# Optimization experiments

Measured on AMD Instinct MI355X. Metric: run time of the kernel, lower is better.

Reference implementation:

```python
import jax, jax.numpy as jnp
import numpy as np

N_NODES = 50000


def _gcn_norm(edge_index, num_nodes):
    # add self loops, compute symmetric normalization D^-1/2 (A+I) D^-1/2
    loops = jnp.arange(num_nodes, dtype=edge_index.dtype)
    row = jnp.concatenate([edge_index[0], loops])
    col = jnp.concatenate([edge_index[1], loops])
    deg = jax.ops.segment_sum(jnp.ones_like(row, dtype=jnp.float32), col,
                              num_segments=num_nodes)
    dinv = jnp.where(deg > 0, jax.lax.rsqrt(deg), 0.0)
    norm = dinv[row] * dinv[col]  # [E']
    return row, col, norm


def _gcn_conv(x, W, b, row, col, norm, num_nodes):
    h = x @ W                       # [N, out] transform first (smaller dim)
    msg = h[row] * norm[:, None]    # gather along source nodes  [E', out]
    agg = jax.ops.segment_sum(msg, col, num_segments=num_nodes)  # scatter-add
    return agg + b


def setup_inputs() -> dict:
    key = jax.random.key(0)
    k1, k2, k3, k4 = jax.random.split(key, 4)
    x = jax.random.normal(k1, (N_NODES, 128), dtype=jnp.float32)
    edge_index = jax.random.randint(k2, (2, 800000), 0, N_NODES, dtype=jnp.int64)
    W1 = jax.random.normal(k3, (128, 128), dtype=jnp.float32) * (1.0 / np.sqrt(128))
    b1 = jnp.zeros((128,), dtype=jnp.float32)
    W2 = jax.random.normal(k4, (128, 16), dtype=jnp.float32) * (1.0 / np.sqrt(128))
    b2 = jnp.zeros((16,), dtype=jnp.float32)
    return {"x": x, "edge_index": edge_index, "W1": W1, "b1": b1, "W2": W2, "b2": b2}


def reference(x, edge_index, W1, b1, W2, b2):
    n = x.shape[0]
    row, col, norm = _gcn_norm(edge_index, n)
    h = _gcn_conv(x, W1, b1, row, col, norm, n)
    h = jax.nn.relu(h)
    h = _gcn_conv(h, W2, b2, row, col, norm, n)
    return jax.nn.log_softmax(h, axis=1)
```

## Files before the change

### kernel.cpp

```cpp
#include <hip/hip_runtime.h>
#include <math.h>

constexpr int N  = 50000;
constexpr int E  = 800000;
constexpr int F1 = 128;
constexpr int F2 = 16;
constexpr int BSHIFT  = 8;
constexpr int NBUCKET = (N + 255) >> BSHIFT;
constexpr int CHUNK   = 2048;
constexpr int CAP     = 6144;

typedef unsigned short ushort_t;
typedef unsigned char  uchar_t;
typedef __bf16 bf16x8 __attribute__((ext_vector_type(8)));
typedef float  f32x4  __attribute__((ext_vector_type(4)));

static __device__ __forceinline__ float blo(unsigned u) { return __uint_as_float(u << 16); }
static __device__ __forceinline__ float bhi(unsigned u) { return __uint_as_float(u & 0xffff0000u); }
static __device__ __forceinline__ ushort_t to_bf(float f) { __bf16 h = (__bf16)f; return *(ushort_t*)&h; }
static __device__ __forceinline__ uchar_t to_fp8(float f) {
    return (uchar_t)(__builtin_amdgcn_cvt_pk_fp8_f32(f, f, 0, false) & 0xff);
}

__global__ __launch_bounds__(256) void k_scatterP(const int* __restrict__ row,
                                                  const int* __restrict__ col,
                                                  int* __restrict__ cursor,
                                                  unsigned* __restrict__ P,
                                                  const float* __restrict__ W1,
                                                  const float* __restrict__ W2,
                                                  ushort_t* __restrict__ W1t,
                                                  ushort_t* __restrict__ W2t) {
    __shared__ int hist[NBUCKET];
    __shared__ int cur[NBUCKET];
    int t = threadIdx.x;
    if (t < NBUCKET) hist[t] = 0;
    __syncthreads();
    int base = blockIdx.x * CHUNK;
#pragma unroll
    for (int i = 0; i < CHUNK / 256; ++i) {
        int e = base + i * 256 + t;
        if (e < E) atomicAdd(&hist[col[e] >> BSHIFT], 1);
    }
    __syncthreads();
    if (t < NBUCKET) cur[t] = t * CAP + atomicAdd(&cursor[t], hist[t]);
    __syncthreads();
#pragma unroll
    for (int i = 0; i < CHUNK / 256; ++i) {
        int e = base + i * 256 + t;
        if (e < E) {
            int c = col[e];
            int pos = atomicAdd(&cur[c >> BSHIFT], 1);
            P[pos] = ((unsigned)row[e] << BSHIFT) | (unsigned)(c & 255);
        }
    }

    int gi = blockIdx.x * 256 + t;
    if (gi < F1 * F1) {
        int k = gi >> 7, n = gi & 127;
        W1t[n * F1 + k] = to_bf(W1[gi]);
    }
    if (gi < F1 * F2) {
        int k = gi >> 4, n = gi & 15;
        W2t[n * F1 + k] = to_bf(W2[gi]);
    }
}

__global__ __launch_bounds__(512) void k_binFinal(const unsigned* __restrict__ P,
                                                  const int* __restrict__ cursor,
                                                  ushort_t* __restrict__ csr16,
                                                  int* __restrict__ seg_start,
                                                  int* __restrict__ counts,
                                                  float* __restrict__ dinv) {
    __shared__ unsigned eb[CAP];
    __shared__ int cnt[256];
    __shared__ int cur[256];
    __shared__ int wtot[4];
    int t = threadIdx.x;
    int b = blockIdx.x;
    int lo = b << BSHIFT;
    int n_nodes = min(256, N - lo);
    int m = cursor[b];
    if (t < 256) cnt[t] = 0;
    __syncthreads();
    const unsigned* Pb = P + (size_t)b * CAP;
    for (int k = t; k < m; k += 512) {
        unsigned u = Pb[k];
        eb[k] = u;
        atomicAdd(&cnt[u & 255], 1);
    }
    __syncthreads();
    int lane = t & 63, wid = t >> 6;
    int v = 0, incl = 0;
    if (t < 256) {
        v = cnt[t];
        incl = v;
#pragma unroll
        for (int d = 1; d < 64; d <<= 1) {
            int u = __shfl_up(incl, d, 64);
            if (lane >= d) incl += u;
        }
        if (lane == 63) wtot[wid] = incl;
    }
    __syncthreads();
    if (t < 256) {
        int wb = 0;
        for (int w = 0; w < wid; ++w) wb += wtot[w];
        int o = b * CAP + wb + incl - v;
        cur[t] = o;
        if (t < n_nodes) {
            seg_start[lo + t] = o;
            counts[lo + t] = v;
            dinv[lo + t] = rsqrtf((float)v + 1.f);
        }
    }
    __syncthreads();
    for (int k = t; k < m; k += 512) {
        unsigned u = eb[k];
        int pos = atomicAdd(&cur[u & 255], 1);
        csr16[pos] = (ushort_t)(u >> BSHIFT);
    }
}

__global__ __launch_bounds__(256) void k_gemm1_mfma(const float* __restrict__ x,
                                                    const ushort_t* __restrict__ W1t,
                                                    const float* __restrict__ dinv,
                                                    uchar_t* __restrict__ h1q) {
    __shared__ ushort_t Wl[F1 * 136];
    int t = threadIdx.x;
    for (int i = t; i < F1 * 16; i += 256) {
        int n = i >> 4, c = (i & 15) * 8;
        *(int4*)&Wl[n * 136 + c] = *(const int4*)&W1t[n * F1 + c];
    }
    __syncthreads();

    int lane = t & 63, wv = t >> 6;
    int quad = lane >> 4, l15 = lane & 15;
    int arow = blockIdx.x * 64 + wv * 16 + l15;
    int rclamp = min(arow, N - 1);
    f32x4 acc[8] = {};

#pragma unroll
    for (int kk = 0; kk < 4; ++kk) {
        int k0 = kk * 32 + quad * 8;
        const float* xp = x + (size_t)rclamp * F1 + k0;
        float4 u0 = *(const float4*)xp;
        float4 u1 = *(const float4*)(xp + 4);
        bf16x8 a;
        a[0] = (__bf16)u0.x; a[1] = (__bf16)u0.y; a[2] = (__bf16)u0.z; a[3] = (__bf16)u0.w;
        a[4] = (__bf16)u1.x; a[5] = (__bf16)u1.y; a[6] = (__bf16)u1.z; a[7] = (__bf16)u1.w;
#pragma unroll
        for (int ct = 0; ct < 8; ++ct) {
            bf16x8 b = *(const bf16x8*)&Wl[(ct * 16 + l15) * 136 + k0];
            acc[ct] = __builtin_amdgcn_mfma_f32_16x16x32_bf16(a, b, acc[ct], 0, 0, 0);
        }
    }

    int orow0 = blockIdx.x * 64 + wv * 16 + quad * 4;
#pragma unroll
    for (int r = 0; r < 4; ++r) {
        int orow = orow0 + r;
        if (orow < N) {
            float d = dinv[orow];
#pragma unroll
            for (int ct = 0; ct < 8; ++ct)
                h1q[(size_t)orow * F1 + ct * 16 + l15] = to_fp8(acc[ct][r] * d);
        }
    }
}

__global__ __launch_bounds__(256) void k_gather1(const uchar_t* __restrict__ h1q,
                                                 const int* __restrict__ seg_start,
                                                 const int* __restrict__ counts,
                                                 const ushort_t* __restrict__ csr16,
                                                 const float* __restrict__ dinv,
                                                 const float* __restrict__ b1,
                                                 ushort_t* __restrict__ h1rb) {
    int c = (blockIdx.x * 256 + threadIdx.x) >> 6;
    int lane = threadIdx.x & 63;
    if (c >= N) return;
    int s = seg_start[c], e = s + counts[c];
    float ax = 0.f, ay = 0.f;
    int k = s;
    for (; k + 4 <= e; k += 4) {
        int r0 = csr16[k], r1 = csr16[k + 1], r2 = csr16[k + 2], r3 = csr16[k + 3];
        unsigned u0 = ((const ushort_t*)(h1q + (size_t)r0 * F1))[lane];
        unsigned u1 = ((const ushort_t*)(h1q + (size_t)r1 * F1))[lane];
        unsigned u2 = ((const ushort_t*)(h1q + (size_t)r2 * F1))[lane];
        unsigned u3 = ((const ushort_t*)(h1q + (size_t)r3 * F1))[lane];
        ax += (__builtin_amdgcn_cvt_f32_fp8(u0, 0) + __builtin_amdgcn_cvt_f32_fp8(u1, 0)) +
              (__builtin_amdgcn_cvt_f32_fp8(u2, 0) + __builtin_amdgcn_cvt_f32_fp8(u3, 0));
        ay += (__builtin_amdgcn_cvt_f32_fp8(u0, 1) + __builtin_amdgcn_cvt_f32_fp8(u1, 1)) +
              (__builtin_amdgcn_cvt_f32_fp8(u2, 1) + __builtin_amdgcn_cvt_f32_fp8(u3, 1));
    }
    for (; k < e; ++k) {
        unsigned u = ((const ushort_t*)(h1q + (size_t)csr16[k] * F1))[lane];
        ax += __builtin_amdgcn_cvt_f32_fp8(u, 0);
        ay += __builtin_amdgcn_cvt_f32_fp8(u, 1);
    }
    unsigned us = ((const ushort_t*)(h1q + (size_t)c * F1))[lane];
    ax += __builtin_amdgcn_cvt_f32_fp8(us, 0);
    ay += __builtin_amdgcn_cvt_f32_fp8(us, 1);
    float dc = dinv[c];
    float2 bb = ((const float2*)b1)[lane];
    float o0 = fmaxf(fmaf(dc, ax, bb.x), 0.f);
    float o1 = fmaxf(fmaf(dc, ay, bb.y), 0.f);
    unsigned pw = (unsigned)to_bf(o0) | ((unsigned)to_bf(o1) << 16);
    ((unsigned*)(h1rb + (size_t)c * F1))[lane] = pw;
}

__global__ __launch_bounds__(256) void k_gemm2_mfma(const ushort_t* __restrict__ h1rb,
                                                    const ushort_t* __restrict__ W2t,
                                                    const float* __restrict__ dinv,
                                                    ushort_t* __restrict__ h2s) {
    int t = threadIdx.x, lane = t & 63, wv = t >> 6;
    int quad = lane >> 4, l15 = lane & 15;
    int arow = blockIdx.x * 64 + wv * 16 + l15;
    int rclamp = min(arow, N - 1);
    f32x4 acc = {};
#pragma unroll
    for (int kk = 0; kk < 4; ++kk) {
        int k0 = kk * 32 + quad * 8;
        bf16x8 a = *(const bf16x8*)(h1rb + (size_t)rclamp * F1 + k0);
        bf16x8 b = *(const bf16x8*)(W2t + l15 * F1 + k0);
        acc = __builtin_amdgcn_mfma_f32_16x16x32_bf16(a, b, acc, 0, 0, 0);
    }
    int orow0 = blockIdx.x * 64 + wv * 16 + quad * 4;
#pragma unroll
    for (int r = 0; r < 4; ++r) {
        int orow = orow0 + r;
        if (orow < N)
            h2s[(size_t)orow * F2 + l15] = to_bf(acc[r] * dinv[orow]);
    }
}

__global__ __launch_bounds__(256) void k_gather2(const ushort_t* __restrict__ h2s,
                                                 const int* __restrict__ seg_start,
                                                 const int* __restrict__ counts,
                                                 const ushort_t* __restrict__ csr16,
                                                 const float* __restrict__ dinv,
                                                 const float* __restrict__ b2,
                                                 float* __restrict__ out) {
    int idx = blockIdx.x * 256 + threadIdx.x;
    int node = idx >> 3, sub = idx & 7;
    if (node >= N) return;
    int s = seg_start[node], e = s + counts[node];
    float ax = 0.f, ay = 0.f;
    int k = s;
    for (; k + 4 <= e; k += 4) {
        int r0 = csr16[k], r1 = csr16[k + 1], r2 = csr16[k + 2], r3 = csr16[k + 3];
        unsigned u0 = ((const unsigned*)(h2s + (size_t)r0 * F2))[sub];
        unsigned u1 = ((const unsigned*)(h2s + (size_t)r1 * F2))[sub];
        unsigned u2 = ((const unsigned*)(h2s + (size_t)r2 * F2))[sub];
        unsigned u3 = ((const unsigned*)(h2s + (size_t)r3 * F2))[sub];
        ax += (blo(u0) + blo(u1)) + (blo(u2) + blo(u3));
        ay += (bhi(u0) + bhi(u1)) + (bhi(u2) + bhi(u3));
    }
    for (; k < e; ++k) {
        unsigned u = ((const unsigned*)(h2s + (size_t)csr16[k] * F2))[sub];
        ax += blo(u);
        ay += bhi(u);
    }
    unsigned us = ((const unsigned*)(h2s + (size_t)node * F2))[sub];
    ax += blo(us);
    ay += bhi(us);
    float dc = dinv[node];
    float2 bb = ((const float2*)b2)[sub];
    float v0 = fmaf(dc, ax, bb.x);
    float v1 = fmaf(dc, ay, bb.y);
    float mx = fmaxf(v0, v1);
#pragma unroll
    for (int m = 1; m < 8; m <<= 1) mx = fmaxf(mx, __shfl_xor(mx, m));
    float sm = expf(v0 - mx) + expf(v1 - mx);
#pragma unroll
    for (int m = 1; m < 8; m <<= 1) sm += __shfl_xor(sm, m);
    float lse = mx + logf(sm);
    float2 o;
    o.x = v0 - lse;
    o.y = v1 - lse;
    ((float2*)(out + (size_t)node * F2))[sub] = o;
}

extern "C" void kernel_launch(void* const* d_in, const int* in_sizes, int n_in,
                              void* d_out, int out_size, void* d_ws, size_t ws_size,
                              hipStream_t stream) {
    const float* x  = (const float*)d_in[0];
    const int*   ei = (const int*)d_in[1];
    const float* W1 = (const float*)d_in[2];
    const float* b1 = (const float*)d_in[3];
    const float* W2 = (const float*)d_in[4];
    const float* b2 = (const float*)d_in[5];
    const int* row = ei;
    const int* col = ei + E;

    char* ws = (char*)d_ws;
    int*      cursor    = (int*)ws;      ws += 256 * 4;
    unsigned* P         = (unsigned*)ws; ws += (size_t)NBUCKET * CAP * 4;
    ushort_t* csr16     = (ushort_t*)ws; ws += (size_t)NBUCKET * CAP * 2;
    int*      seg_start = (int*)ws;      ws += (size_t)N * 4;
    int*      counts    = (int*)ws;      ws += (size_t)N * 4;
    float*    dinv      = (float*)ws;    ws += (size_t)N * 4;
    ushort_t* W1t       = (ushort_t*)ws; ws += (size_t)F1 * F1 * 2;
    ushort_t* W2t       = (ushort_t*)ws; ws += (size_t)F2 * F1 * 2;
    uchar_t*  h1q       = (uchar_t*)ws;  ws += (size_t)N * F1;
    ushort_t* h1rb      = (ushort_t*)ws; ws += (size_t)N * F1 * 2;
    ushort_t* h2s       = (ushort_t*)ws; ws += (size_t)N * F2 * 2;

    hipMemsetAsync(cursor, 0, 256 * 4, stream);

    int nbin_blocks = (E + CHUNK - 1) / CHUNK;
    k_scatterP<<<nbin_blocks, 256, 0, stream>>>(row, col, cursor, P, W1, W2, W1t, W2t);
    k_binFinal<<<NBUCKET, 512, 0, stream>>>(P, cursor, csr16, seg_start, counts, dinv);

    k_gemm1_mfma<<<(N + 63) / 64, 256, 0, stream>>>(x, W1t, dinv, h1q);
    k_gather1<<<((size_t)N * 64 + 255) / 256, 256, 0, stream>>>(h1q, seg_start, counts, csr16,
                                                                dinv, b1, h1rb);

    k_gemm2_mfma<<<(N + 63) / 64, 256, 0, stream>>>(h1rb, W2t, dinv, h2s);
    k_gather2<<<((size_t)N * 8 + 255) / 256, 256, 0, stream>>>(h2s, seg_start, counts, csr16,
                                                               dinv, b2, (float*)d_out);
}
```

Before: 163.7 us.

## Fuse edge scatter with GEMM1 and gather1 with GEMM2, move dinv to gather

GEMM1 no longer depends on dinv, so it runs in the same launch as the edge-bucketing scatter, with extra blocks each transposing W1 into LDS themselves. The source-side dinv scale moves into gather1, which now does a per-edge fma with dinv[row]. Gather1 is fused with GEMM2: each block aggregates 16 nodes into LDS and one wave does the 128x16 MFMA, so the bf16 h1 intermediate is never written to memory. This saves two launches and a full N x 128 round trip, at the cost of an extra dinv gather per edge, a single-wave MFMA tail per block, and the fp8 quantization now happening before the dinv scaling.

```diff
diff --git a/kernel.cpp b/kernel.cpp
--- a/kernel.cpp
+++ b/kernel.cpp
@@ -9,6 +9,8 @@
 constexpr int NBUCKET = (N + 255) >> BSHIFT;
 constexpr int CHUNK   = 2048;
 constexpr int CAP     = 6144;
+constexpr int SBLK    = (E + CHUNK - 1) / CHUNK;
+constexpr int GBLK    = 391;
 
 typedef unsigned short ushort_t;
 typedef unsigned char  uchar_t;
@@ -21,47 +23,91 @@
 static __device__ __forceinline__ uchar_t to_fp8(float f) {
     return (uchar_t)(__builtin_amdgcn_cvt_pk_fp8_f32(f, f, 0, false) & 0xff);
 }
-
-__global__ __launch_bounds__(256) void k_scatterP(const int* __restrict__ row,
-                                                  const int* __restrict__ col,
-                                                  int* __restrict__ cursor,
-                                                  unsigned* __restrict__ P,
-                                                  const float* __restrict__ W1,
-                                                  const float* __restrict__ W2,
-                                                  ushort_t* __restrict__ W1t,
-                                                  ushort_t* __restrict__ W2t) {
-    __shared__ int hist[NBUCKET];
-    __shared__ int cur[NBUCKET];
+static __device__ __forceinline__ float fp8lo(unsigned u) { return __builtin_amdgcn_cvt_f32_fp8(u, 0); }
+static __device__ __forceinline__ float fp8hi(unsigned u) { return __builtin_amdgcn_cvt_f32_fp8(u, 1); }
+
+__global__ __launch_bounds__(256) void k_scatterP_gemm1(const int* __restrict__ row,
+                                                        const int* __restrict__ col,
+                                                        int* __restrict__ cursor,
+                                                        unsigned* __restrict__ P,
+                                                        const float* __restrict__ x,
+                                                        const float* __restrict__ W1,
+                                                        uchar_t* __restrict__ h1q) {
+    __shared__ ushort_t Wl[F1 * 136];
     int t = threadIdx.x;
-    if (t < NBUCKET) hist[t] = 0;
-    __syncthreads();
-    int base = blockIdx.x * CHUNK;
-#pragma unroll
-    for (int i = 0; i < CHUNK / 256; ++i) {
-        int e = base + i * 256 + t;
-        if (e < E) atomicAdd(&hist[col[e] >> BSHIFT], 1);
-    }
-    __syncthreads();
-    if (t < NBUCKET) cur[t] = t * CAP + atomicAdd(&cursor[t], hist[t]);
-    __syncthreads();
-#pragma unroll
-    for (int i = 0; i < CHUNK / 256; ++i) {
-        int e = base + i * 256 + t;
-        if (e < E) {
-            int c = col[e];
-            int pos = atomicAdd(&cur[c >> BSHIFT], 1);
-            P[pos] = ((unsigned)row[e] << BSHIFT) | (unsigned)(c & 255);
-        }
-    }
-
-    int gi = blockIdx.x * 256 + t;
-    if (gi < F1 * F1) {
-        int k = gi >> 7, n = gi & 127;
-        W1t[n * F1 + k] = to_bf(W1[gi]);
-    }
-    if (gi < F1 * F2) {
-        int k = gi >> 4, n = gi & 15;
-        W2t[n * F1 + k] = to_bf(W2[gi]);
+
+    if (blockIdx.x < SBLK) {
+        int* hist = (int*)Wl;
+        int* cur  = hist + NBUCKET;
+        if (t < NBUCKET) hist[t] = 0;
+        __syncthreads();
+        int base = blockIdx.x * CHUNK;
+#pragma unroll
+        for (int i = 0; i < CHUNK / 256; ++i) {
+            int e = base + i * 256 + t;
+            if (e < E) atomicAdd(&hist[col[e] >> BSHIFT], 1);
+        }
+        __syncthreads();
+        if (t < NBUCKET) cur[t] = t * CAP + atomicAdd(&cursor[t], hist[t]);
+        __syncthreads();
+#pragma unroll
+        for (int i = 0; i < CHUNK / 256; ++i) {
+            int e = base + i * 256 + t;
+            if (e < E) {
+                int c = col[e];
+                int pos = atomicAdd(&cur[c >> BSHIFT], 1);
+                P[pos] = ((unsigned)row[e] << BSHIFT) | (unsigned)(c & 255);
+            }
+        }
+        return;
+    }
+
+    int gb = blockIdx.x - SBLK;
+    {
+        int n = t & 127, kh = t >> 7;
+#pragma unroll
+        for (int j = 0; j < 8; ++j) {
+            int k0 = (kh * 8 + j) * 8;
+            bf16x8 w;
+#pragma unroll
+            for (int i2 = 0; i2 < 8; ++i2) w[i2] = (__bf16)W1[(k0 + i2) * F1 + n];
+            *(bf16x8*)&Wl[n * 136 + k0] = w;
+        }
+    }
+    __syncthreads();
+
+    int lane = t & 63, wv = t >> 6;
+    int quad = lane >> 4, l15 = lane & 15;
+#pragma unroll 1
+    for (int tile = gb * 2; tile < gb * 2 + 2; ++tile) {
+        int arow = tile * 64 + wv * 16 + l15;
+        int rclamp = min(arow, N - 1);
+        f32x4 acc[8] = {};
+#pragma unroll
+        for (int kk = 0; kk < 4; ++kk) {
+            int k0 = kk * 32 + quad * 8;
+            const float* xp = x + (size_t)rclamp * F1 + k0;
+            float4 u0 = *(const float4*)xp;
+            float4 u1 = *(const float4*)(xp + 4);
+            bf16x8 a;
+            a[0] = (__bf16)u0.x; a[1] = (__bf16)u0.y; a[2] = (__bf16)u0.z; a[3] = (__bf16)u0.w;
+            a[4] = (__bf16)u1.x; a[5] = (__bf16)u1.y; a[6] = (__bf16)u1.z; a[7] = (__bf16)u1.w;
+#pragma unroll
+            for (int ct = 0; ct < 8; ++ct) {
+                bf16x8 b = *(const bf16x8*)&Wl[(ct * 16 + l15) * 136 + k0];
+                acc[ct] = __builtin_amdgcn_mfma_f32_16x16x32_bf16(a, b, acc[ct], 0, 0, 0);
+            }
+        }
+        int orow0 = tile * 64 + wv * 16 + quad * 4;
+#pragma unroll
+        for (int r = 0; r < 4; ++r) {
+            int orow = orow0 + r;
+            if (orow < N) {
+#pragma unroll
+                for (int ct = 0; ct < 8; ++ct)
+                    h1q[(size_t)orow * F1 + ct * 16 + l15] = to_fp8(acc[ct][r]);
+            }
+        }
     }
 }
 
@@ -121,115 +167,82 @@
     }
 }
 
-__global__ __launch_bounds__(256) void k_gemm1_mfma(const float* __restrict__ x,
-                                                    const ushort_t* __restrict__ W1t,
-                                                    const float* __restrict__ dinv,
-                                                    uchar_t* __restrict__ h1q) {
-    __shared__ ushort_t Wl[F1 * 136];
+__global__ __launch_bounds__(256) void k_gather1_gemm2(const uchar_t* __restrict__ h1q,
+                                                       const int* __restrict__ seg_start,
+                                                       const int* __restrict__ counts,
+                                                       const ushort_t* __restrict__ csr16,
+                                                       const float* __restrict__ dinv,
+                                                       const float* __restrict__ W2,
+                                                       const float* __restrict__ b1,
+                                                       ushort_t* __restrict__ h2s) {
+    __shared__ ushort_t W2l[F2 * 136];
+    __shared__ ushort_t T[16 * 136];
+    __shared__ float dv[16];
     int t = threadIdx.x;
-    for (int i = t; i < F1 * 16; i += 256) {
-        int n = i >> 4, c = (i & 15) * 8;
-        *(int4*)&Wl[n * 136 + c] = *(const int4*)&W1t[n * F1 + c];
-    }
-    __syncthreads();
-
+    for (int i = t; i < F1 * F2; i += 256) {
+        int k = i >> 4, n = i & 15;
+        W2l[n * 136 + k] = to_bf(W2[i]);
+    }
     int lane = t & 63, wv = t >> 6;
-    int quad = lane >> 4, l15 = lane & 15;
-    int arow = blockIdx.x * 64 + wv * 16 + l15;
-    int rclamp = min(arow, N - 1);
-    f32x4 acc[8] = {};
-
-#pragma unroll
-    for (int kk = 0; kk < 4; ++kk) {
-        int k0 = kk * 32 + quad * 8;
-        const float* xp = x + (size_t)rclamp * F1 + k0;
-        float4 u0 = *(const float4*)xp;
-        float4 u1 = *(const float4*)(xp + 4);
-        bf16x8 a;
-        a[0] = (__bf16)u0.x; a[1] = (__bf16)u0.y; a[2] = (__bf16)u0.z; a[3] = (__bf16)u0.w;
-        a[4] = (__bf16)u1.x; a[5] = (__bf16)u1.y; a[6] = (__bf16)u1.z; a[7] = (__bf16)u1.w;
-#pragma unroll
-        for (int ct = 0; ct < 8; ++ct) {
-            bf16x8 b = *(const bf16x8*)&Wl[(ct * 16 + l15) * 136 + k0];
-            acc[ct] = __builtin_amdgcn_mfma_f32_16x16x32_bf16(a, b, acc[ct], 0, 0, 0);
-        }
-    }
-
-    int orow0 = blockIdx.x * 64 + wv * 16 + quad * 4;
-#pragma unroll
-    for (int r = 0; r < 4; ++r) {
-        int orow = orow0 + r;
-        if (orow < N) {
-            float d = dinv[orow];
-#pragma unroll
-            for (int ct = 0; ct < 8; ++ct)
-                h1q[(size_t)orow * F1 + ct * 16 + l15] = to_fp8(acc[ct][r] * d);
-        }
-    }
-}
-
-__global__ __launch_bounds__(256) void k_gather1(const uchar_t* __restrict__ h1q,
-                                                 const int* __restrict__ seg_start,
-                                                 const int* __restrict__ counts,
-                                                 const ushort_t* __restrict__ csr16,
-                                                 const float* __restrict__ dinv,
-                                                 const float* __restrict__ b1,
-                                                 ushort_t* __restrict__ h1rb) {
-    int c = (blockIdx.x * 256 + threadIdx.x) >> 6;
-    int lane = threadIdx.x & 63;
-    if (c >= N) return;
-    int s = seg_start[c], e = s + counts[c];
-    float ax = 0.f, ay = 0.f;
-    int k = s;
-    for (; k + 4 <= e; k += 4) {
-        int r0 = csr16[k], r1 = csr16[k + 1], r2 = csr16[k + 2], r3 = csr16[k + 3];
-        unsigned u0 = ((const ushort_t*)(h1q + (size_t)r0 * F1))[lane];
-        unsigned u1 = ((const ushort_t*)(h1q + (size_t)r1 * F1))[lane];
-        unsigned u2 = ((const ushort_t*)(h1q + (size_t)r2 * F1))[lane];
-        unsigned u3 = ((const ushort_t*)(h1q + (size_t)r3 * F1))[lane];
-        ax += (__builtin_amdgcn_cvt_f32_fp8(u0, 0) + __builtin_amdgcn_cvt_f32_fp8(u1, 0)) +
-              (__builtin_amdgcn_cvt_f32_fp8(u2, 0) + __builtin_amdgcn_cvt_f32_fp8(u3, 0));
-        ay += (__builtin_amdgcn_cvt_f32_fp8(u0, 1) + __builtin_amdgcn_cvt_f32_fp8(u1, 1)) +
-              (__builtin_amdgcn_cvt_f32_fp8(u2, 1) + __builtin_amdgcn_cvt_f32_fp8(u3, 1));
-    }
-    for (; k < e; ++k) {
-        unsigned u = ((const ushort_t*)(h1q + (size_t)csr16[k] * F1))[lane];
-        ax += __builtin_amdgcn_cvt_f32_fp8(u, 0);
-        ay += __builtin_amdgcn_cvt_f32_fp8(u, 1);
-    }
-    unsigned us = ((const ushort_t*)(h1q + (size_t)c * F1))[lane];
-    ax += __builtin_amdgcn_cvt_f32_fp8(us, 0);
-    ay += __builtin_amdgcn_cvt_f32_fp8(us, 1);
-    float dc = dinv[c];
     float2 bb = ((const float2*)b1)[lane];
-    float o0 = fmaxf(fmaf(dc, ax, bb.x), 0.f);
-    float o1 = fmaxf(fmaf(dc, ay, bb.y), 0.f);
-    unsigned pw = (unsigned)to_bf(o0) | ((unsigned)to_bf(o1) << 16);
-    ((unsigned*)(h1rb + (size_t)c * F1))[lane] = pw;
-}
-
-__global__ __launch_bounds__(256) void k_gemm2_mfma(const ushort_t* __restrict__ h1rb,
-                                                    const ushort_t* __restrict__ W2t,
-                                                    const float* __restrict__ dinv,
-                                                    ushort_t* __restrict__ h2s) {
-    int t = threadIdx.x, lane = t & 63, wv = t >> 6;
-    int quad = lane >> 4, l15 = lane & 15;
-    int arow = blockIdx.x * 64 + wv * 16 + l15;
-    int rclamp = min(arow, N - 1);
-    f32x4 acc = {};
-#pragma unroll
-    for (int kk = 0; kk < 4; ++kk) {
-        int k0 = kk * 32 + quad * 8;
-        bf16x8 a = *(const bf16x8*)(h1rb + (size_t)rclamp * F1 + k0);
-        bf16x8 b = *(const bf16x8*)(W2t + l15 * F1 + k0);
-        acc = __builtin_amdgcn_mfma_f32_16x16x32_bf16(a, b, acc, 0, 0, 0);
-    }
-    int orow0 = blockIdx.x * 64 + wv * 16 + quad * 4;
-#pragma unroll
-    for (int r = 0; r < 4; ++r) {
-        int orow = orow0 + r;
-        if (orow < N)
-            h2s[(size_t)orow * F2 + l15] = to_bf(acc[r] * dinv[orow]);
+    int nbase = blockIdx.x * 16;
+
+#pragma unroll 1
+    for (int i = 0; i < 4; ++i) {
+        int nl = wv * 4 + i;
+        int c = nbase + nl;
+        unsigned pw = 0u;
+        float dc = 0.f;
+        if (c < N) {
+            dc = dinv[c];
+            int s = seg_start[c], e = s + counts[c];
+            float ax = 0.f, ay = 0.f;
+            int k = s;
+            for (; k + 4 <= e; k += 4) {
+                int r0 = csr16[k], r1 = csr16[k + 1], r2 = csr16[k + 2], r3 = csr16[k + 3];
+                float d0 = dinv[r0], d1 = dinv[r1], d2 = dinv[r2], d3 = dinv[r3];
+                unsigned u0 = ((const ushort_t*)(h1q + (size_t)r0 * F1))[lane];
+                unsigned u1 = ((const ushort_t*)(h1q + (size_t)r1 * F1))[lane];
+                unsigned u2 = ((const ushort_t*)(h1q + (size_t)r2 * F1))[lane];
+                unsigned u3 = ((const ushort_t*)(h1q + (size_t)r3 * F1))[lane];
+                ax = fmaf(d0, fp8lo(u0), ax); ay = fmaf(d0, fp8hi(u0), ay);
+                ax = fmaf(d1, fp8lo(u1), ax); ay = fmaf(d1, fp8hi(u1), ay);
+                ax = fmaf(d2, fp8lo(u2), ax); ay = fmaf(d2, fp8hi(u2), ay);
+                ax = fmaf(d3, fp8lo(u3), ax); ay = fmaf(d3, fp8hi(u3), ay);
+            }
+            for (; k < e; ++k) {
+                int r0 = csr16[k];
+                float d0 = dinv[r0];
+                unsigned u0 = ((const ushort_t*)(h1q + (size_t)r0 * F1))[lane];
+                ax = fmaf(d0, fp8lo(u0), ax); ay = fmaf(d0, fp8hi(u0), ay);
+            }
+            unsigned us = ((const ushort_t*)(h1q + (size_t)c * F1))[lane];
+            ax = fmaf(dc, fp8lo(us), ax); ay = fmaf(dc, fp8hi(us), ay);
+            float o0 = fmaxf(fmaf(dc, ax, bb.x), 0.f);
+            float o1 = fmaxf(fmaf(dc, ay, bb.y), 0.f);
+            pw = (unsigned)to_bf(o0) | ((unsigned)to_bf(o1) << 16);
+        }
+        *(unsigned*)&T[nl * 136 + lane * 2] = pw;
+        if (lane == 0) dv[nl] = dc;
+    }
+    __syncthreads();
+
+    if (wv == 0) {
+        int quad = lane >> 4, l15 = lane & 15;
+        f32x4 acc = {};
+#pragma unroll
+        for (int kk = 0; kk < 4; ++kk) {
+            int k0 = kk * 32 + quad * 8;
+            bf16x8 a = *(const bf16x8*)&T[l15 * 136 + k0];
+            bf16x8 b = *(const bf16x8*)&W2l[l15 * 136 + k0];
+            acc = __builtin_amdgcn_mfma_f32_16x16x32_bf16(a, b, acc, 0, 0, 0);
+        }
+#pragma unroll
+        for (int r = 0; r < 4; ++r) {
+            int rw = quad * 4 + r;
+            int gn = nbase + rw;
+            if (gn < N) h2s[(size_t)gn * F2 + l15] = to_bf(acc[r] * dv[rw]);
+        }
     }
 }
 
@@ -299,23 +312,15 @@
     int*      seg_start = (int*)ws;      ws += (size_t)N * 4;
     int*      counts    = (int*)ws;      ws += (size_t)N * 4;
     float*    dinv      = (float*)ws;    ws += (size_t)N * 4;
-    ushort_t* W1t       = (ushort_t*)ws; ws += (size_t)F1 * F1 * 2;
-    ushort_t* W2t       = (ushort_t*)ws; ws += (size_t)F2 * F1 * 2;
     uchar_t*  h1q       = (uchar_t*)ws;  ws += (size_t)N * F1;
-    ushort_t* h1rb      = (ushort_t*)ws; ws += (size_t)N * F1 * 2;
     ushort_t* h2s       = (ushort_t*)ws; ws += (size_t)N * F2 * 2;
 
     hipMemsetAsync(cursor, 0, 256 * 4, stream);
 
-    int nbin_blocks = (E + CHUNK - 1) / CHUNK;
-    k_scatterP<<<nbin_blocks, 256, 0, stream>>>(row, col, cursor, P, W1, W2, W1t, W2t);
+    k_scatterP_gemm1<<<SBLK + GBLK, 256, 0, stream>>>(row, col, cursor, P, x, W1, h1q);
     k_binFinal<<<NBUCKET, 512, 0, stream>>>(P, cursor, csr16, seg_start, counts, dinv);
-
-    k_gemm1_mfma<<<(N + 63) / 64, 256, 0, stream>>>(x, W1t, dinv, h1q);
-    k_gather1<<<((size_t)N * 64 + 255) / 256, 256, 0, stream>>>(h1q, seg_start, counts, csr16,
-                                                                dinv, b1, h1rb);
-
-    k_gemm2_mfma<<<(N + 63) / 64, 256, 0, stream>>>(h1rb, W2t, dinv, h2s);
+    k_gather1_gemm2<<<(N + 15) / 16, 256, 0, stream>>>(h1q, seg_start, counts, csr16,
+                                                       dinv, W2, b1, h2s);
     k_gather2<<<((size_t)N * 8 + 255) / 256, 256, 0, stream>>>(h2s, seg_start, counts, csr16,
                                                                dinv, b2, (float*)d_out);
 }
```

After: 160.1 us. 1.02x faster.
